# Kernel tuning notes

Hardware: AMD Instinct MI355X
Metric: run time of the kernel (lower is better)

The kernel has to match this reference:

```python
import jax, jax.numpy as jnp
import numpy as np

B, N, D = 16, 8192, 384   # examples, sentences per example, embedding dim
KN = 16                   # neighbors per node (kNN degree)
K, H, STEPS = 8, 128, 3   # coin dim, hidden dim, walk steps


def setup_inputs() -> dict:
    key = jax.random.key(0)
    ks = jax.random.split(key, 12)
    s = 0.02
    return {
        "sent_embs": jax.random.normal(ks[0], (B, N, D), dtype=jnp.float32),
        "q_embs": jax.random.normal(ks[1], (B, D), dtype=jnp.float32),
        "neighbors": jax.random.randint(ks[2], (B, N, KN), 0, N, dtype=jnp.int32),
        # coin_net: Linear(2D->H), ReLU, Linear(H->K)
        "coin_w1": jax.random.normal(ks[3], (2 * D, H), dtype=jnp.float32) * s,
        "coin_b1": jnp.zeros((H,), dtype=jnp.float32),
        "coin_w2": jax.random.normal(ks[4], (H, K), dtype=jnp.float32) * s,
        "coin_b2": jnp.zeros((K,), dtype=jnp.float32),
        # path_net: Linear(D+K+D->H), ReLU, Linear(H->1)
        "path_w1": jax.random.normal(ks[5], (D + K + D, H), dtype=jnp.float32) * s,
        "path_b1": jnp.zeros((H,), dtype=jnp.float32),
        "path_w2": jax.random.normal(ks[6], (H, 1), dtype=jnp.float32) * s,
        "path_b2": jnp.zeros((1,), dtype=jnp.float32),
    }


def _mlp(x, w1, b1, w2, b2):
    return jax.nn.relu(x @ w1 + b1) @ w2 + b2


def _forward(sent_embs, q_embs, neighbors,
             coin_w1, coin_b1, coin_w2, coin_b2,
             path_w1, path_b1, path_w2, path_b2):
    b, n, d = sent_embs.shape
    k = coin_w2.shape[1]
    q_bcast = jnp.broadcast_to(q_embs[:, None, :], (b, n, d))

    # coin amplitudes per node: [B, N, K]
    amps = _mlp(jnp.concatenate([sent_embs, q_bcast], axis=-1),
                coin_w1, coin_b1, coin_w2, coin_b2)

    # initial uniform walk state: 1/sqrt(N*K)
    state = jnp.full((b, n, k), 1.0 / np.sqrt(n * k), dtype=sent_embs.dtype)

    # adjacency = self-loop + edges row -> neighbors[row]; A @ X == X + masked neighbor gather-sum
    valid = (neighbors >= 0) & (neighbors < n)           # [B, N, KN]
    safe_nbrs = jnp.where(valid, neighbors, 0)
    batch_idx = jnp.arange(b)[:, None, None]

    for _ in range(STEPS):
        ns = state * amps                                # coin step
        gathered = ns[batch_idx, safe_nbrs]              # [B, N, KN, K]
        gathered = jnp.where(valid[..., None], gathered, 0.0)
        ns = ns + gathered.sum(axis=2)                   # sparse.mm(A, ns)
        norm = jnp.linalg.norm(ns.reshape(b, -1), axis=1)[:, None, None]
        state = ns / jnp.where(norm > 0, norm, 1.0)      # renormalize (guard norm==0)

    path_in = jnp.concatenate([sent_embs, state, q_bcast], axis=-1)  # [B, N, D+K+D]
    logits = _mlp(path_in, path_w1, path_b1, path_w2, path_b2)[..., 0]  # [B, N]
    return logits


def reference(sent_embs, q_embs, neighbors,
              coin_w1, coin_b1, coin_w2, coin_b2,
              path_w1, path_b1, path_w2, path_b2):
    return _forward(sent_embs, q_embs, neighbors,
                    coin_w1, coin_b1, coin_w2, coin_b2,
                    path_w1, path_b1, path_w2, path_b2)
```

## Files before the change

kernel.cpp:

```cpp
#include <hip/hip_runtime.h>

#define B_SZ 16
#define N_SZ 8192
#define D_SZ 384
#define KN_SZ 16
#define K_SZ 8
#define H_SZ 128
#define M_TOTAL (B_SZ * N_SZ)
#define KSTEPS 12
#define MT64 (M_TOTAL / 64)
#define LDSA_STRIDE 400

typedef short short8 __attribute__((ext_vector_type(8)));
typedef short short4v __attribute__((ext_vector_type(4)));
typedef float floatx4 __attribute__((ext_vector_type(4)));

__device__ __forceinline__ unsigned short f2bf(float f) {
    unsigned u = __builtin_bit_cast(unsigned, f);
    u += 0x7FFFu + ((u >> 16) & 1u);
    return (unsigned short)(u >> 16);
}
__device__ __forceinline__ float bf2f(unsigned short b) {
    unsigned u = ((unsigned)b) << 16;
    return __builtin_bit_cast(float, u);
}
__device__ __forceinline__ unsigned pkbf(float a, float b) {
    unsigned r;
    asm("v_cvt_pk_bf16_f32 %0, %1, %2" : "=v"(r) : "v"(a), "v"(b));
    return r;
}

__global__ void prep_kernel(const float* __restrict__ q_embs,
                            const float* __restrict__ coin_w1,
                            const float* __restrict__ coin_b1,
                            const float* __restrict__ path_w1,
                            const float* __restrict__ path_b1,
                            unsigned short* __restrict__ wswz,
                            float* __restrict__ qcoin, float* __restrict__ qpath,
                            float* __restrict__ norms) {
    int blk = blockIdx.x;
    int t = threadIdx.x;
    if (blk < 384) {
        int f = blk * 256 + t;
        int j  = f & 7;
        int l  = (f >> 3) & 63;
        int ss = (f >> 9) % KSTEPS;
        int ct = f / (KSTEPS * 512);
        int k = ss * 32 + ((l >> 4) << 3) + j;
        int n = ct * 16 + (l & 15);
        float v = (n < H_SZ) ? coin_w1[k * H_SZ + n]
                             : path_w1[k * H_SZ + (n - H_SZ)];
        wswz[f] = f2bf(v);
    } else if (blk == 384) {
        if (t < B_SZ) norms[t] = 0.f;
    } else {
        int b = blk - 385;
        const float* q = q_embs + b * D_SZ;
        if (t < H_SZ) {
            float acc = coin_b1[t];
            for (int d = 0; d < D_SZ; d++)
                acc += q[d] * coin_w1[(D_SZ + d) * H_SZ + t];
            qcoin[b * H_SZ + t] = acc;
        } else if (t < 2 * H_SZ) {
            int h = t - H_SZ;
            float acc = path_b1[h];
            for (int d = 0; d < D_SZ; d++)
                acc += q[d] * path_w1[(D_SZ + K_SZ + d) * H_SZ + h];
            qpath[b * H_SZ + h] = acc;
        }
    }
}

__global__ __launch_bounds__(256)
void gemm_fused(const float* __restrict__ sent,
                const unsigned short* __restrict__ wswz,
                const float* __restrict__ qcoin,
                const float* __restrict__ coin_w2,
                const float* __restrict__ coin_b2,
                unsigned short* __restrict__ hpathB,
                float* __restrict__ amps,
                float* __restrict__ z0) {
    __shared__ __align__(16) short als[64 * LDSA_STRIDE];
    const int tid = threadIdx.x;
    const int wave = tid >> 6, lane = tid & 63;
    const int m_lane = lane & 15, quad = lane >> 4;
    const int mt = blockIdx.x;
    const int b = mt >> 7;

    const float* abase = sent + (size_t)mt * 64 * D_SZ;
#pragma unroll
    for (int g = 0; g < 3; g++) {
        float4 v[8];
#pragma unroll
        for (int u = 0; u < 8; u++)
            v[u] = *(const float4*)(abase + (size_t)((g * 8 + u) * 256 + tid) * 4);
#pragma unroll
        for (int u = 0; u < 8; u++) {
            int e4 = (g * 8 + u) * 256 + tid;
            int row = e4 / 96;
            int c4  = e4 - row * 96;
            int2 p;
            p.x = (int)pkbf(v[u].x, v[u].y);
            p.y = (int)pkbf(v[u].z, v[u].w);
            *(int2*)&als[row * LDSA_STRIDE + c4 * 4] = p;
        }
    }
    __syncthreads();

    const unsigned short* wbase = wswz + (size_t)wave * 4 * KSTEPS * 512 + lane * 8;
    floatx4 acc[4][4];
#pragma unroll
    for (int rt = 0; rt < 4; rt++)
#pragma unroll
        for (int c = 0; c < 4; c++) acc[rt][c] = (floatx4){0.f, 0.f, 0.f, 0.f};

#pragma unroll
    for (int s = 0; s < KSTEPS; s++) {
        short8 bf[4];
#pragma unroll
        for (int c = 0; c < 4; c++)
            bf[c] = *(const short8*)(wbase + (size_t)(c * KSTEPS + s) * 512);
        short8 af[4];
#pragma unroll
        for (int rt = 0; rt < 4; rt++)
            af[rt] = *(const short8*)&als[(rt * 16 + m_lane) * LDSA_STRIDE + s * 32 + quad * 8];
#pragma unroll
        for (int rt = 0; rt < 4; rt++)
#pragma unroll
            for (int c = 0; c < 4; c++)
                acc[rt][c] = __builtin_amdgcn_mfma_f32_16x16x32_bf16(af[rt], bf[c], acc[rt][c], 0, 0, 0);
    }

    if (wave >= 2) {
        const int colw = (wave & 1) * 64;
#pragma unroll
        for (int rt = 0; rt < 4; rt++) {
            int mt16 = mt * 4 + rt;
#pragma unroll
            for (int c = 0; c < 4; c++) {
                int col = colw + c * 16 + m_lane;
                int2 p;
                p.x = (int)pkbf(acc[rt][c][0], acc[rt][c][1]);
                p.y = (int)pkbf(acc[rt][c][2], acc[rt][c][3]);
                *(int2*)(hpathB + (size_t)mt16 * 2048 + col * 16 + quad * 4) = p;
            }
        }
    }
    __syncthreads();

    float* hs  = (float*)als;
    float* w2s = hs + 64 * 132;
    if (wave < 2) {
        const int colw = wave * 64;
        float qc[4];
#pragma unroll
        for (int c = 0; c < 4; c++)
            qc[c] = qcoin[b * H_SZ + colw + c * 16 + m_lane];
#pragma unroll
        for (int rt = 0; rt < 4; rt++)
#pragma unroll
            for (int c = 0; c < 4; c++) {
                int colj = colw + c * 16 + m_lane;
#pragma unroll
                for (int j = 0; j < 4; j++) {
                    int row = rt * 16 + quad * 4 + j;
                    float hv = acc[rt][c][j] + qc[c];
                    hs[row * 132 + colj] = hv > 0.f ? hv : 0.f;
                }
            }
    }
    for (int i = tid; i < H_SZ * K_SZ; i += 256) w2s[i] = coin_w2[i];
    __syncthreads();

    {
        const int r = tid >> 2;
        const int kk = (tid & 3) * 2;
        float a0 = coin_b2[kk], a1 = coin_b2[kk + 1];
#pragma unroll 8
        for (int c = 0; c < H_SZ; c++) {
            float hv = hs[r * 132 + c];
            float2 w = *(const float2*)&w2s[c * 8 + kk];
            a0 += hv * w.x; a1 += hv * w.y;
        }
        const size_t m = (size_t)mt * 64 + r;
        const float c0 = 1.0f / 256.0f;
        *(float2*)(amps + m * 8 + kk) = make_float2(a0, a1);
        *(float2*)(z0   + m * 8 + kk) = make_float2(a0 * c0, a1 * c0);
    }
}

__global__ __launch_bounds__(256)
void walk_step(const float* __restrict__ z,
               const int* __restrict__ neighbors,
               const float* __restrict__ amps,
               float* __restrict__ outz,
               float* __restrict__ norms, int last) {
    const int g = blockIdx.x * 256 + threadIdx.x;
    const int m = g >> 1, half = g & 1;
    const int b = m >> 13;
    const size_t nbase = (size_t)b << 13;
    const int off = half * 4;

    float4 v = *(const float4*)(z + (size_t)m * 8 + off);
    int nbr[KN_SZ];
    const int4* nb4 = (const int4*)(neighbors + (size_t)m * KN_SZ);
#pragma unroll
    for (int i = 0; i < 4; i++) *(int4*)&nbr[i * 4] = nb4[i];
#pragma unroll
    for (int i = 0; i < KN_SZ; i++) {
        int nn = nbr[i];
        if (nn >= 0 && nn < N_SZ) {
            float4 gv = *(const float4*)(z + (nbase + nn) * 8 + off);
            v.x += gv.x; v.y += gv.y; v.z += gv.z; v.w += gv.w;
        }
    }
    if (!last) {
        float4 a = *(const float4*)(amps + (size_t)m * 8 + off);
        v.x *= a.x; v.y *= a.y; v.z *= a.z; v.w *= a.w;
        *(float4*)(outz + (size_t)m * 8 + off) = v;
    } else {
        *(float4*)(outz + (size_t)m * 8 + off) = v;
        float ss = v.x * v.x + v.y * v.y + v.z * v.z + v.w * v.w;
#pragma unroll
        for (int o = 32; o > 0; o >>= 1) ss += __shfl_down(ss, o);
        __shared__ float blocksum;
        if (threadIdx.x == 0) blocksum = 0.f;
        __syncthreads();
        if ((threadIdx.x & 63) == 0) atomicAdd(&blocksum, ss);
        __syncthreads();
        if (threadIdx.x == 0) atomicAdd(&norms[b], blocksum);
    }
}

__global__ __launch_bounds__(256)
void logits_kernel(const unsigned short* __restrict__ hpathB,
                   const float* __restrict__ qpath,
                   const float* __restrict__ u2,
                   const float* __restrict__ norms,
                   const float* __restrict__ path_w1,
                   const float* __restrict__ path_w2,
                   const float* __restrict__ path_b2,
                   float* __restrict__ out) {
    __shared__ float w1t[H_SZ * K_SZ];
    __shared__ float w2s[H_SZ];
    __shared__ float qps[H_SZ];
    const int tid = threadIdx.x;
    const int m = blockIdx.x * 256 + tid;
    const int b = (blockIdx.x * 256) >> 13;
    for (int i = tid; i < K_SZ * H_SZ; i += 256) {
        int h = i >> 3, j = i & 7;
        w1t[i] = path_w1[(D_SZ + j) * H_SZ + h];
    }
    if (tid < H_SZ) { w2s[tid] = path_w2[tid]; qps[tid] = qpath[b * H_SZ + tid]; }
    __syncthreads();

    float ssq = norms[b];
    float inv = ssq > 0.f ? rsqrtf(ssq) : 1.0f;
    float st[K_SZ];
    {
        float4 s0 = *(const float4*)(u2 + (size_t)m * 8);
        float4 s1 = *(const float4*)(u2 + (size_t)m * 8 + 4);
        st[0] = s0.x * inv; st[1] = s0.y * inv; st[2] = s0.z * inv; st[3] = s0.w * inv;
        st[4] = s1.x * inv; st[5] = s1.y * inv; st[6] = s1.z * inv; st[7] = s1.w * inv;
    }

    const unsigned short* hb = hpathB + (size_t)(m >> 4) * 2048 + (m & 15);
    float acc = path_b2[0];
    for (int h = 0; h < H_SZ; h++) {
        float hv = bf2f(hb[h * 16]) + qps[h];
        float4 wa = *(const float4*)&w1t[h * 8];
        float4 wb = *(const float4*)&w1t[h * 8 + 4];
        hv += st[0]*wa.x + st[1]*wa.y + st[2]*wa.z + st[3]*wa.w
            + st[4]*wb.x + st[5]*wb.y + st[6]*wb.z + st[7]*wb.w;
        hv = hv > 0.f ? hv : 0.f;
        acc += hv * w2s[h];
    }
    out[m] = acc;
}

extern "C" void kernel_launch(void* const* d_in, const int* in_sizes, int n_in,
                              void* d_out, int out_size, void* d_ws, size_t ws_size,
                              hipStream_t stream) {
    const float* sent      = (const float*)d_in[0];
    const float* q_embs    = (const float*)d_in[1];
    const int*   neighbors = (const int*)d_in[2];
    const float* coin_w1   = (const float*)d_in[3];
    const float* coin_b1   = (const float*)d_in[4];
    const float* coin_w2   = (const float*)d_in[5];
    const float* coin_b2   = (const float*)d_in[6];
    const float* path_w1   = (const float*)d_in[7];
    const float* path_b1   = (const float*)d_in[8];
    const float* path_w2   = (const float*)d_in[9];
    const float* path_b2   = (const float*)d_in[10];
    float* out = (float*)d_out;

    char* ws = (char*)d_ws;
    unsigned short* wswz = (unsigned short*)ws;
    float* qcoin = (float*)(ws + 196608);
    float* qpath = (float*)(ws + 204800);
    float* norms = (float*)(ws + 212992);
    unsigned short* hpathB = (unsigned short*)(ws + 213248);
    float* amps = (float*)(ws + 33767680);
    float* zA   = (float*)(ws + 37961984);
    float* zB   = (float*)(ws + 42156288);

    prep_kernel<<<401, 256, 0, stream>>>(q_embs, coin_w1, coin_b1, path_w1, path_b1,
                                         wswz, qcoin, qpath, norms);
    gemm_fused<<<MT64, 256, 0, stream>>>(sent, wswz, qcoin, coin_w2, coin_b2,
                                         hpathB, amps, zA);
    walk_step<<<2 * M_TOTAL / 256, 256, 0, stream>>>(zA, neighbors, amps, zB, norms, 0);
    walk_step<<<2 * M_TOTAL / 256, 256, 0, stream>>>(zB, neighbors, amps, zA, norms, 0);
    walk_step<<<2 * M_TOTAL / 256, 256, 0, stream>>>(zA, neighbors, amps, zB, norms, 1);
    logits_kernel<<<M_TOTAL / 256, 256, 0, stream>>>(hpathB, qpath, zB, norms,
                                                     path_w1, path_w2, path_b2, out);
}
```

Baseline: 406.9 us.

## Store hpath row-major, split logits across 8 lanes, drop z0 buffer

```diff
diff --git a/kernel.cpp b/kernel.cpp
--- a/kernel.cpp
+++ b/kernel.cpp
@@ -77,9 +77,8 @@
                 const float* __restrict__ qcoin,
                 const float* __restrict__ coin_w2,
                 const float* __restrict__ coin_b2,
-                unsigned short* __restrict__ hpathB,
-                float* __restrict__ amps,
-                float* __restrict__ z0) {
+                unsigned short* __restrict__ hpath,
+                float* __restrict__ amps) {
     __shared__ __align__(16) short als[64 * LDSA_STRIDE];
     const int tid = threadIdx.x;
     const int wave = tid >> 6, lane = tid & 63;
@@ -133,18 +132,18 @@
 
     if (wave >= 2) {
         const int colw = (wave & 1) * 64;
-#pragma unroll
-        for (int rt = 0; rt < 4; rt++) {
-            int mt16 = mt * 4 + rt;
+        unsigned short* hrow = hpath + (size_t)mt * 64 * H_SZ;
+#pragma unroll
+        for (int rt = 0; rt < 4; rt++)
 #pragma unroll
             for (int c = 0; c < 4; c++) {
                 int col = colw + c * 16 + m_lane;
-                int2 p;
-                p.x = (int)pkbf(acc[rt][c][0], acc[rt][c][1]);
-                p.y = (int)pkbf(acc[rt][c][2], acc[rt][c][3]);
-                *(int2*)(hpathB + (size_t)mt16 * 2048 + col * 16 + quad * 4) = p;
+#pragma unroll
+                for (int j = 0; j < 4; j++) {
+                    int row = rt * 16 + quad * 4 + j;
+                    hrow[row * H_SZ + col] = f2bf(acc[rt][c][j]);
+                }
             }
-        }
     }
     __syncthreads();
 
@@ -183,9 +182,7 @@
             a0 += hv * w.x; a1 += hv * w.y;
         }
         const size_t m = (size_t)mt * 64 + r;
-        const float c0 = 1.0f / 256.0f;
         *(float2*)(amps + m * 8 + kk) = make_float2(a0, a1);
-        *(float2*)(z0   + m * 8 + kk) = make_float2(a0 * c0, a1 * c0);
     }
 }
 
@@ -194,7 +191,7 @@
                const int* __restrict__ neighbors,
                const float* __restrict__ amps,
                float* __restrict__ outz,
-               float* __restrict__ norms, int last) {
+               float* __restrict__ norms, int last, float presc) {
     const int g = blockIdx.x * 256 + threadIdx.x;
     const int m = g >> 1, half = g & 1;
     const int b = m >> 13;
@@ -214,6 +211,7 @@
             v.x += gv.x; v.y += gv.y; v.z += gv.z; v.w += gv.w;
         }
     }
+    v.x *= presc; v.y *= presc; v.z *= presc; v.w *= presc;
     if (!last) {
         float4 a = *(const float4*)(amps + (size_t)m * 8 + off);
         v.x *= a.x; v.y *= a.y; v.z *= a.z; v.w *= a.w;
@@ -233,7 +231,7 @@
 }
 
 __global__ __launch_bounds__(256)
-void logits_kernel(const unsigned short* __restrict__ hpathB,
+void logits_kernel(const unsigned short* __restrict__ hpath,
                    const float* __restrict__ qpath,
                    const float* __restrict__ u2,
                    const float* __restrict__ norms,
@@ -241,19 +239,25 @@
                    const float* __restrict__ path_w2,
                    const float* __restrict__ path_b2,
                    float* __restrict__ out) {
-    __shared__ float w1t[H_SZ * K_SZ];
-    __shared__ float w2s[H_SZ];
-    __shared__ float qps[H_SZ];
+    __shared__ float w1t2[H_SZ * K_SZ];
+    __shared__ float w2s2[H_SZ];
+    __shared__ float qps2[H_SZ];
     const int tid = threadIdx.x;
-    const int m = blockIdx.x * 256 + tid;
-    const int b = (blockIdx.x * 256) >> 13;
-    for (int i = tid; i < K_SZ * H_SZ; i += 256) {
-        int h = i >> 3, j = i & 7;
-        w1t[i] = path_w1[(D_SZ + j) * H_SZ + h];
-    }
-    if (tid < H_SZ) { w2s[tid] = path_w2[tid]; qps[tid] = qpath[b * H_SZ + tid]; }
+    const int mbase = blockIdx.x * 32;
+    const int b = mbase >> 13;
+    for (int i2 = tid; i2 < H_SZ * K_SZ; i2 += 256) {
+        int i = i2 >> 6, sg = (i2 >> 3) & 7, j = i2 & 7;
+        w1t2[i2] = path_w1[(D_SZ + j) * H_SZ + (sg * 16 + i)];
+    }
+    if (tid < H_SZ) {
+        int idx = (tid & 15) * 8 + (tid >> 4);
+        w2s2[idx] = path_w2[tid];
+        qps2[idx] = qpath[b * H_SZ + tid];
+    }
     __syncthreads();
 
+    const int m = mbase + (tid >> 3);
+    const int seg = tid & 7;
     float ssq = norms[b];
     float inv = ssq > 0.f ? rsqrtf(ssq) : 1.0f;
     float st[K_SZ];
@@ -263,19 +267,26 @@
         st[0] = s0.x * inv; st[1] = s0.y * inv; st[2] = s0.z * inv; st[3] = s0.w * inv;
         st[4] = s1.x * inv; st[5] = s1.y * inv; st[6] = s1.z * inv; st[7] = s1.w * inv;
     }
-
-    const unsigned short* hb = hpathB + (size_t)(m >> 4) * 2048 + (m & 15);
-    float acc = path_b2[0];
-    for (int h = 0; h < H_SZ; h++) {
-        float hv = bf2f(hb[h * 16]) + qps[h];
-        float4 wa = *(const float4*)&w1t[h * 8];
-        float4 wb = *(const float4*)&w1t[h * 8 + 4];
+    const unsigned short* hb = hpath + (size_t)m * H_SZ + seg * 16;
+    short8 hv0 = *(const short8*)hb;
+    short8 hv1 = *(const short8*)(hb + 8);
+
+    float acc = 0.f;
+#pragma unroll
+    for (int i = 0; i < 16; i++) {
+        unsigned short hraw = (unsigned short)(i < 8 ? hv0[i] : hv1[i - 8]);
+        float hv = bf2f(hraw) + qps2[i * 8 + seg];
+        float4 wa = *(const float4*)&w1t2[i * 64 + seg * 8];
+        float4 wb = *(const float4*)&w1t2[i * 64 + seg * 8 + 4];
         hv += st[0]*wa.x + st[1]*wa.y + st[2]*wa.z + st[3]*wa.w
             + st[4]*wb.x + st[5]*wb.y + st[6]*wb.z + st[7]*wb.w;
         hv = hv > 0.f ? hv : 0.f;
-        acc += hv * w2s[h];
-    }
-    out[m] = acc;
+        acc += hv * w2s2[i * 8 + seg];
+    }
+    acc += __shfl_xor(acc, 4);
+    acc += __shfl_xor(acc, 2);
+    acc += __shfl_xor(acc, 1);
+    if (seg == 0) out[m] = acc + path_b2[0];
 }
 
 extern "C" void kernel_launch(void* const* d_in, const int* in_sizes, int n_in,
@@ -299,7 +310,7 @@
     float* qcoin = (float*)(ws + 196608);
     float* qpath = (float*)(ws + 204800);
     float* norms = (float*)(ws + 212992);
-    unsigned short* hpathB = (unsigned short*)(ws + 213248);
+    unsigned short* hpath = (unsigned short*)(ws + 213248);
     float* amps = (float*)(ws + 33767680);
     float* zA   = (float*)(ws + 37961984);
     float* zB   = (float*)(ws + 42156288);
@@ -307,10 +318,10 @@
     prep_kernel<<<401, 256, 0, stream>>>(q_embs, coin_w1, coin_b1, path_w1, path_b1,
                                          wswz, qcoin, qpath, norms);
     gemm_fused<<<MT64, 256, 0, stream>>>(sent, wswz, qcoin, coin_w2, coin_b2,
-                                         hpathB, amps, zA);
-    walk_step<<<2 * M_TOTAL / 256, 256, 0, stream>>>(zA, neighbors, amps, zB, norms, 0);
-    walk_step<<<2 * M_TOTAL / 256, 256, 0, stream>>>(zB, neighbors, amps, zA, norms, 0);
-    walk_step<<<2 * M_TOTAL / 256, 256, 0, stream>>>(zA, neighbors, amps, zB, norms, 1);
-    logits_kernel<<<M_TOTAL / 256, 256, 0, stream>>>(hpathB, qpath, zB, norms,
-                                                     path_w1, path_w2, path_b2, out);
-}
+                                         hpath, amps);
+    walk_step<<<2 * M_TOTAL / 256, 256, 0, stream>>>(amps, neighbors, amps, zB, norms, 0, 1.0f / 256.0f);
+    walk_step<<<2 * M_TOTAL / 256, 256, 0, stream>>>(zB, neighbors, amps, zA, norms, 0, 1.0f);
+    walk_step<<<2 * M_TOTAL / 256, 256, 0, stream>>>(zA, neighbors, amps, zB, norms, 1, 1.0f);
+    logits_kernel<<<M_TOTAL / 32, 256, 0, stream>>>(hpath, qpath, zB, norms,
+                                                    path_w1, path_w2, path_b2, out);
+}
```

Result: no change. 412.7 us (+1.4%).

## Double-buffer GEMM A-tile loads, drop z0 buffer, split logits H-loop across lanes

Applied to the files above, without the earlier changes.

```diff
diff --git a/kernel.cpp b/kernel.cpp
--- a/kernel.cpp
+++ b/kernel.cpp
@@ -9,7 +9,9 @@
 #define M_TOTAL (B_SZ * N_SZ)
 #define KSTEPS 12
 #define MT64 (M_TOTAL / 64)
-#define LDSA_STRIDE 400
+#define CK 128
+#define LDSB_STRIDE 144
+#define HS_STRIDE 130
 
 typedef short short8 __attribute__((ext_vector_type(8)));
 typedef short short4v __attribute__((ext_vector_type(4)));
@@ -78,34 +80,21 @@
                 const float* __restrict__ coin_w2,
                 const float* __restrict__ coin_b2,
                 unsigned short* __restrict__ hpathB,
-                float* __restrict__ amps,
-                float* __restrict__ z0) {
-    __shared__ __align__(16) short als[64 * LDSA_STRIDE];
+                float* __restrict__ amps) {
+    __shared__ __align__(16) short als[2 * 64 * LDSB_STRIDE];
+    __shared__ float w2s[H_SZ * K_SZ];
+    short* buf0 = als;
+    short* buf1 = als + 64 * LDSB_STRIDE;
     const int tid = threadIdx.x;
     const int wave = tid >> 6, lane = tid & 63;
     const int m_lane = lane & 15, quad = lane >> 4;
     const int mt = blockIdx.x;
     const int b = mt >> 7;
-
     const float* abase = sent + (size_t)mt * 64 * D_SZ;
-#pragma unroll
-    for (int g = 0; g < 3; g++) {
-        float4 v[8];
-#pragma unroll
-        for (int u = 0; u < 8; u++)
-            v[u] = *(const float4*)(abase + (size_t)((g * 8 + u) * 256 + tid) * 4);
-#pragma unroll
-        for (int u = 0; u < 8; u++) {
-            int e4 = (g * 8 + u) * 256 + tid;
-            int row = e4 / 96;
-            int c4  = e4 - row * 96;
-            int2 p;
-            p.x = (int)pkbf(v[u].x, v[u].y);
-            p.y = (int)pkbf(v[u].z, v[u].w);
-            *(int2*)&als[row * LDSA_STRIDE + c4 * 4] = p;
-        }
-    }
-    __syncthreads();
+    const int row8 = tid >> 5;
+    const int c4   = tid & 31;
+
+    for (int i = tid; i < H_SZ * K_SZ; i += 256) w2s[i] = coin_w2[i];
 
     const unsigned short* wbase = wswz + (size_t)wave * 4 * KSTEPS * 512 + lane * 8;
     floatx4 acc[4][4];
@@ -114,22 +103,56 @@
 #pragma unroll
         for (int c = 0; c < 4; c++) acc[rt][c] = (floatx4){0.f, 0.f, 0.f, 0.f};
 
-#pragma unroll
-    for (int s = 0; s < KSTEPS; s++) {
-        short8 bf[4];
-#pragma unroll
-        for (int c = 0; c < 4; c++)
-            bf[c] = *(const short8*)(wbase + (size_t)(c * KSTEPS + s) * 512);
-        short8 af[4];
-#pragma unroll
-        for (int rt = 0; rt < 4; rt++)
-            af[rt] = *(const short8*)&als[(rt * 16 + m_lane) * LDSA_STRIDE + s * 32 + quad * 8];
-#pragma unroll
-        for (int rt = 0; rt < 4; rt++)
-#pragma unroll
-            for (int c = 0; c < 4; c++)
-                acc[rt][c] = __builtin_amdgcn_mfma_f32_16x16x32_bf16(af[rt], bf[c], acc[rt][c], 0, 0, 0);
-    }
+    float4 v[8];
+
+#define STAGE_LOAD(CHUNK)                                                        \
+    _Pragma("unroll")                                                            \
+    for (int u = 0; u < 8; u++)                                                  \
+        v[u] = *(const float4*)(abase + (size_t)(row8 + u * 8) * D_SZ +          \
+                                (CHUNK) * CK + c4 * 4);
+
+#define STAGE_STORE(BUF)                                                         \
+    _Pragma("unroll")                                                            \
+    for (int u = 0; u < 8; u++) {                                                \
+        int2 p;                                                                  \
+        p.x = (int)pkbf(v[u].x, v[u].y);                                         \
+        p.y = (int)pkbf(v[u].z, v[u].w);                                         \
+        *(int2*)&(BUF)[(row8 + u * 8) * LDSB_STRIDE + c4 * 4] = p;               \
+    }
+
+#define MMA_CHUNK(BUF, CHUNK)                                                    \
+    _Pragma("unroll")                                                            \
+    for (int sl = 0; sl < 4; sl++) {                                             \
+        const int s = (CHUNK) * 4 + sl;                                          \
+        short8 bfr[4];                                                           \
+        _Pragma("unroll")                                                        \
+        for (int cc = 0; cc < 4; cc++)                                           \
+            bfr[cc] = *(const short8*)(wbase + (size_t)(cc * KSTEPS + s) * 512); \
+        short8 af[4];                                                            \
+        _Pragma("unroll")                                                        \
+        for (int rt = 0; rt < 4; rt++)                                           \
+            af[rt] = *(const short8*)&(BUF)[(rt * 16 + m_lane) * LDSB_STRIDE +   \
+                                            sl * 32 + quad * 8];                 \
+        _Pragma("unroll")                                                        \
+        for (int rt = 0; rt < 4; rt++)                                           \
+            _Pragma("unroll")                                                    \
+            for (int cc = 0; cc < 4; cc++)                                       \
+                acc[rt][cc] = __builtin_amdgcn_mfma_f32_16x16x32_bf16(           \
+                    af[rt], bfr[cc], acc[rt][cc], 0, 0, 0);                      \
+    }
+
+    STAGE_LOAD(0);
+    STAGE_STORE(buf0);
+    __syncthreads();
+    STAGE_LOAD(1);
+    MMA_CHUNK(buf0, 0);
+    STAGE_STORE(buf1);
+    __syncthreads();
+    STAGE_LOAD(2);
+    MMA_CHUNK(buf1, 1);
+    STAGE_STORE(buf0);
+    __syncthreads();
+    MMA_CHUNK(buf0, 2);
 
     if (wave >= 2) {
         const int colw = (wave & 1) * 64;
@@ -148,8 +171,7 @@
     }
     __syncthreads();
 
-    float* hs  = (float*)als;
-    float* w2s = hs + 64 * 132;
+    float* hs = (float*)als;
     if (wave < 2) {
         const int colw = wave * 64;
         float qc[4];
@@ -165,11 +187,10 @@
                 for (int j = 0; j < 4; j++) {
                     int row = rt * 16 + quad * 4 + j;
                     float hv = acc[rt][c][j] + qc[c];
-                    hs[row * 132 + colj] = hv > 0.f ? hv : 0.f;
+                    hs[row * HS_STRIDE + colj] = hv > 0.f ? hv : 0.f;
                 }
             }
     }
-    for (int i = tid; i < H_SZ * K_SZ; i += 256) w2s[i] = coin_w2[i];
     __syncthreads();
 
     {
@@ -178,15 +199,16 @@
         float a0 = coin_b2[kk], a1 = coin_b2[kk + 1];
 #pragma unroll 8
         for (int c = 0; c < H_SZ; c++) {
-            float hv = hs[r * 132 + c];
+            float hv = hs[r * HS_STRIDE + c];
             float2 w = *(const float2*)&w2s[c * 8 + kk];
             a0 += hv * w.x; a1 += hv * w.y;
         }
         const size_t m = (size_t)mt * 64 + r;
-        const float c0 = 1.0f / 256.0f;
         *(float2*)(amps + m * 8 + kk) = make_float2(a0, a1);
-        *(float2*)(z0   + m * 8 + kk) = make_float2(a0 * c0, a1 * c0);
-    }
+    }
+#undef STAGE_LOAD
+#undef STAGE_STORE
+#undef MMA_CHUNK
 }
 
 __global__ __launch_bounds__(256)
@@ -194,7 +216,7 @@
                const int* __restrict__ neighbors,
                const float* __restrict__ amps,
                float* __restrict__ outz,
-               float* __restrict__ norms, int last) {
+               float* __restrict__ norms, int last, float presc) {
     const int g = blockIdx.x * 256 + threadIdx.x;
     const int m = g >> 1, half = g & 1;
     const int b = m >> 13;
@@ -214,6 +236,7 @@
             v.x += gv.x; v.y += gv.y; v.z += gv.z; v.w += gv.w;
         }
     }
+    v.x *= presc; v.y *= presc; v.z *= presc; v.w *= presc;
     if (!last) {
         float4 a = *(const float4*)(amps + (size_t)m * 8 + off);
         v.x *= a.x; v.y *= a.y; v.z *= a.z; v.w *= a.w;
@@ -241,19 +264,25 @@
                    const float* __restrict__ path_w2,
                    const float* __restrict__ path_b2,
                    float* __restrict__ out) {
-    __shared__ float w1t[H_SZ * K_SZ];
-    __shared__ float w2s[H_SZ];
-    __shared__ float qps[H_SZ];
+    __shared__ float w1t[4 * 260];
+    __shared__ float w2sp[4 * 33];
+    __shared__ float qps[4 * 33];
     const int tid = threadIdx.x;
-    const int m = blockIdx.x * 256 + tid;
-    const int b = (blockIdx.x * 256) >> 13;
-    for (int i = tid; i < K_SZ * H_SZ; i += 256) {
-        int h = i >> 3, j = i & 7;
-        w1t[i] = path_w1[(D_SZ + j) * H_SZ + h];
-    }
-    if (tid < H_SZ) { w2s[tid] = path_w2[tid]; qps[tid] = qpath[b * H_SZ + tid]; }
-    __syncthreads();
-
+    const int mbase = blockIdx.x * 64;
+    const int b = mbase >> 13;
+    for (int i2 = tid; i2 < H_SZ * K_SZ; i2 += 256) {
+        int h = i2 >> 3, j = i2 & 7;
+        w1t[(h >> 5) * 260 + (h & 31) * 8 + j] = path_w1[(D_SZ + j) * H_SZ + h];
+    }
+    if (tid < H_SZ) {
+        int idx = (tid >> 5) * 33 + (tid & 31);
+        w2sp[idx] = path_w2[tid];
+        qps[idx]  = qpath[b * H_SZ + tid];
+    }
+    __syncthreads();
+
+    const int m = mbase + (tid >> 2);
+    const int seg = tid & 3;
     float ssq = norms[b];
     float inv = ssq > 0.f ? rsqrtf(ssq) : 1.0f;
     float st[K_SZ];
@@ -263,19 +292,26 @@
         st[0] = s0.x * inv; st[1] = s0.y * inv; st[2] = s0.z * inv; st[3] = s0.w * inv;
         st[4] = s1.x * inv; st[5] = s1.y * inv; st[6] = s1.z * inv; st[7] = s1.w * inv;
     }
-
     const unsigned short* hb = hpathB + (size_t)(m >> 4) * 2048 + (m & 15);
-    float acc = path_b2[0];
-    for (int h = 0; h < H_SZ; h++) {
-        float hv = bf2f(hb[h * 16]) + qps[h];
-        float4 wa = *(const float4*)&w1t[h * 8];
-        float4 wb = *(const float4*)&w1t[h * 8 + 4];
+    const float* w1b = &w1t[seg * 260];
+    const float* w2b = &w2sp[seg * 33];
+    const float* qpb = &qps[seg * 33];
+    const int hseg = seg * 32;
+
+    float acc = 0.f;
+#pragma unroll 8
+    for (int i = 0; i < 32; i++) {
+        float hv = bf2f(hb[(hseg + i) * 16]) + qpb[i];
+        float4 wa = *(const float4*)&w1b[i * 8];
+        float4 wb = *(const float4*)&w1b[i * 8 + 4];
         hv += st[0]*wa.x + st[1]*wa.y + st[2]*wa.z + st[3]*wa.w
             + st[4]*wb.x + st[5]*wb.y + st[6]*wb.z + st[7]*wb.w;
         hv = hv > 0.f ? hv : 0.f;
-        acc += hv * w2s[h];
-    }
-    out[m] = acc;
+        acc += hv * w2b[i];
+    }
+    acc += __shfl_xor(acc, 1);
+    acc += __shfl_xor(acc, 2);
+    if (seg == 0) out[m] = acc + path_b2[0];
 }
 
 extern "C" void kernel_launch(void* const* d_in, const int* in_sizes, int n_in,
@@ -307,10 +343,10 @@
     prep_kernel<<<401, 256, 0, stream>>>(q_embs, coin_w1, coin_b1, path_w1, path_b1,
                                          wswz, qcoin, qpath, norms);
     gemm_fused<<<MT64, 256, 0, stream>>>(sent, wswz, qcoin, coin_w2, coin_b2,
-                                         hpathB, amps, zA);
-    walk_step<<<2 * M_TOTAL / 256, 256, 0, stream>>>(zA, neighbors, amps, zB, norms, 0);
-    walk_step<<<2 * M_TOTAL / 256, 256, 0, stream>>>(zB, neighbors, amps, zA, norms, 0);
-    walk_step<<<2 * M_TOTAL / 256, 256, 0, stream>>>(zA, neighbors, amps, zB, norms, 1);
-    logits_kernel<<<M_TOTAL / 256, 256, 0, stream>>>(hpathB, qpath, zB, norms,
-                                                     path_w1, path_w2, path_b2, out);
-}
+                                         hpathB, amps);
+    walk_step<<<2 * M_TOTAL / 256, 256, 0, stream>>>(amps, neighbors, amps, zB, norms, 0, 1.0f / 256.0f);
+    walk_step<<<2 * M_TOTAL / 256, 256, 0, stream>>>(zB, neighbors, amps, zA, norms, 0, 1.0f);
+    walk_step<<<2 * M_TOTAL / 256, 256, 0, stream>>>(zA, neighbors, amps, zB, norms, 1, 1.0f);
+    logits_kernel<<<M_TOTAL / 64, 256, 0, stream>>>(hpathB, qpath, zB, norms,
+                                                    path_w1, path_w2, path_b2, out);
+}
```

New measurement: 402.9 us. Within noise of the previous version (-1.0%).
